# Optimization experiments

Measured on AMD Instinct MI355X. Metric: run time of the kernel, lower is better.

## Reference

```python
import jax, jax.numpy as jnp
import numpy as np

D_MODEL = 1024
N_HEADS = 16
HEAD_DIM = D_MODEL // N_HEADS


def _rotary_tables(seq_len, dim):
    # sin/cos tables: (seq_len, dim//2)
    pos = jnp.arange(seq_len, dtype=jnp.float32)[:, None]
    freqs = 1.0 / 10000.0 ** (jnp.arange(0, dim, 2, dtype=jnp.float32) / dim)
    angles = pos * freqs
    return jnp.sin(angles), jnp.cos(angles)


def _apply_rotary(x, sin, cos):
    # x: (B, H, N, head_dim); sin/cos: (N, head_dim//2) broadcast over B,H
    d_half = x.shape[-1] // 2
    x1, x2 = x[..., :d_half], x[..., d_half:]
    return jnp.concatenate([x1 * cos - x2 * sin, x1 * sin + x2 * cos], axis=-1)


def setup_inputs() -> dict:
    key = jax.random.key(0)
    k_x, k_q, k_k, k_v, k_o = jax.random.split(key, 5)
    B, N = 4, 2048
    scale = 1.0 / np.sqrt(D_MODEL)
    return {
        "x": jax.random.normal(k_x, (B, N, D_MODEL), dtype=jnp.float32),
        "Wq": jax.random.normal(k_q, (D_MODEL, D_MODEL), dtype=jnp.float32) * scale,
        "Wk": jax.random.normal(k_k, (D_MODEL, D_MODEL), dtype=jnp.float32) * scale,
        "Wv": jax.random.normal(k_v, (D_MODEL, D_MODEL), dtype=jnp.float32) * scale,
        "Wo": jax.random.normal(k_o, (D_MODEL, D_MODEL), dtype=jnp.float32) * scale,
    }


def reference(x, Wq, Wk, Wv, Wo):
    B, N, _ = x.shape
    # nn.Linear(d, d, bias=False): y = x @ W.T ; view+transpose -> (B, H, N, hd)
    def proj(W):
        return jnp.einsum('bnd,ed->bne', x, W).reshape(B, N, N_HEADS, HEAD_DIM).transpose(0, 2, 1, 3)

    Q, K, V = proj(Wq), proj(Wk), proj(Wv)
    sin, cos = _rotary_tables(N, HEAD_DIM)
    Q = _apply_rotary(Q, sin, cos)
    K = _apply_rotary(K, sin, cos)

    # SDPA (non-causal, dropout=0): softmax(Q K^T / sqrt(hd)) V
    scores = jnp.einsum('bhqd,bhkd->bhqk', Q, K) / jnp.sqrt(jnp.asarray(HEAD_DIM, x.dtype))
    attn = jax.nn.softmax(scores, axis=-1)
    out = jnp.einsum('bhqk,bhkd->bhqd', attn, V)  # (B, H, N, hd)
    out = out.transpose(0, 2, 1, 3).reshape(B, N, D_MODEL)
    return jnp.einsum('bnd,ed->bne', out, Wo)
```

## Files before the change

kernel.cpp:

```cpp
#include <hip/hip_runtime.h>
#include <stdint.h>

#define SEQ    2048
#define DMODEL 1024
#define NHEADS 16
#define HDIM   64
#define BATCH  4
#define MTOT   (BATCH*SEQ)

typedef __attribute__((ext_vector_type(8)))  short s16x8;
typedef __attribute__((ext_vector_type(4)))  short s16x4;
typedef __attribute__((ext_vector_type(4)))  float f32x4;
typedef __attribute__((ext_vector_type(16))) float f32x16;

#define OFF_SIN  ((size_t)0)
#define OFF_COS  ((size_t)262144)
#define OFF_XHI  ((size_t)524288)
#define OFF_WQH  ((size_t)34078720)
#define OFF_WKH  ((size_t)38273024)
#define OFF_WVH  ((size_t)42467328)
#define OFF_WOH  ((size_t)46661632)
#define OFF_QR   ((size_t)50855936)
#define OFF_KR   ((size_t)67633152)
#define OFF_VT   ((size_t)84410368)
#define OFF_AHI  ((size_t)101187584)

#define QSCALE 0.18033688011112042f

__device__ __forceinline__ uint16_t f2bf(float f){
  union{float f;uint32_t u;}v; v.f=f;
  uint32_t r=v.u+0x7fffu+((v.u>>16)&1u);
  return (uint16_t)(r>>16);
}
__device__ __forceinline__ float bf2f(uint16_t u){
  union{uint32_t u;float f;}v; v.u=((uint32_t)u)<<16; return v.f;
}

__device__ __forceinline__ void async16(void* lds, const void* g){
  __builtin_amdgcn_global_load_lds(
    (const __attribute__((address_space(1))) void*)g,
    (__attribute__((address_space(3))) void*)lds, 16, 0, 0);
}

__device__ __forceinline__ float fexp2(float x){
#if __has_builtin(__builtin_amdgcn_exp2f)
  return __builtin_amdgcn_exp2f(x);
#else
  float r; asm("v_exp_f32 %0, %1" : "=v"(r) : "v"(x)); return r;
#endif
}
__device__ __forceinline__ float frcp(float x){
#if __has_builtin(__builtin_amdgcn_rcpf)
  return __builtin_amdgcn_rcpf(x);
#else
  float r; asm("v_rcp_f32 %0, %1" : "=v"(r) : "v"(x)); return r;
#endif
}
__device__ __forceinline__ void plswap(unsigned a, unsigned b, unsigned &o0, unsigned &o1){
#if __has_builtin(__builtin_amdgcn_permlane32_swap)
  auto r = __builtin_amdgcn_permlane32_swap(a, b, false, false);
  o0 = (unsigned)r[0]; o1 = (unsigned)r[1];
#else
  unsigned ax = (unsigned)__shfl_xor((int)a, 32, 64);
  unsigned bx = (unsigned)__shfl_xor((int)b, 32, 64);
  bool hi = (threadIdx.x & 32) != 0;
  o0 = hi ? bx : a;
  o1 = hi ? b  : ax;
#endif
}

__global__ __launch_bounds__(256) void prep_k(
  const float* __restrict__ x,
  const float* __restrict__ Wq, const float* __restrict__ Wk,
  const float* __restrict__ Wv, const float* __restrict__ Wo,
  uint16_t* __restrict__ xhi, uint16_t* __restrict__ wqh, uint16_t* __restrict__ wkh,
  uint16_t* __restrict__ wvh, uint16_t* __restrict__ woh,
  float* __restrict__ st, float* __restrict__ ct)
{
  int b = blockIdx.x;
  if (b < 12288){
    const float* s; uint16_t* d; int i;
    if (b < 8192){ s = x; d = xhi; i = b*256 + threadIdx.x; }
    else {
      int wsel = (b - 8192) >> 10;
      int lb   = (b - 8192) & 1023;
      s = wsel==0? Wq : wsel==1? Wk : wsel==2? Wv : Wo;
      d = wsel==0? wqh: wsel==1? wkh: wsel==2? wvh: woh;
      i = lb*256 + threadIdx.x;
    }
    f32x4 v = *(const f32x4*)(s + (size_t)i*4);
    s16x4 vh;
    #pragma unroll
    for(int r=0;r<4;r++) vh[r] = (short)f2bf(v[r]);
    *(s16x4*)(d + (size_t)i*4) = vh;
  } else {
    int i = (b - 12288)*256 + threadIdx.x;
    int n = i>>5, j = i&31;
    float freq = powf(10000.f, -(float)j/32.f);
    float ang = (float)n*freq;
    st[i] = sinf(ang);
    ct[i] = cosf(ang);
  }
}

__device__ __forceinline__ void gemm_mainloop64(
  const uint16_t* __restrict__ A, const uint16_t* __restrict__ B,
  int m0, int e0, char* lA, char* lB, f32x4 acc[4][4])
{
  const int t = threadIdx.x;
  const int lane = t & 63;
  const int wr = t>>7, wc = (t>>6)&1;
  const int lq = lane&15, lg = lane>>4;
  const int rowA = wr*64 + lq;
  const int rowB = wc*64 + lq;

  int dbyte[4], srow[4], sbyte[4];
  #pragma unroll
  for (int s=0;s<4;s++){
    int d = s*4096 + t*16;
    int r = d>>7, c = (d>>4)&7;
    dbyte[s]=d; srow[s]=r; sbyte[s]=(c ^ (r&7))*16;
  }
  int chh[2];
  #pragma unroll
  for (int kh=0;kh<2;kh++) chh[kh] = (((kh<<2)|lg) ^ (lq&7))*16;
  const bool oddw = ((t>>6) & 1) != 0;
  const int cF = oddw ? chh[1] : chh[0];
  const int cS = oddw ? chh[0] : chh[1];

  const char* Ab = (const char*)A;
  const char* Bb = (const char*)B;

  for (int k0=0; k0<DMODEL; k0+=64){
    #pragma unroll
    for (int s=0;s<4;s++){
      async16(lA + dbyte[s], Ab + (size_t)(m0+srow[s])*2048 + k0*2 + sbyte[s]);
      async16(lB + dbyte[s], Bb + (size_t)(e0+srow[s])*2048 + k0*2 + sbyte[s]);
    }
    __syncthreads();
    #pragma unroll
    for (int ph=0; ph<2; ++ph){
      const int ch = ph ? cS : cF;
      s16x8 af[4], bfr[4];
      #pragma unroll
      for (int mi=0;mi<4;mi++) af[mi]  = *(const s16x8*)(lA + (rowA+mi*16)*128 + ch);
      #pragma unroll
      for (int ni=0;ni<4;ni++) bfr[ni] = *(const s16x8*)(lB + (rowB+ni*16)*128 + ch);
      __builtin_amdgcn_s_setprio(1);
      #pragma unroll
      for (int mi=0;mi<4;mi++){
        #pragma unroll
        for (int ni=0;ni<4;ni++)
          acc[mi][ni] = __builtin_amdgcn_mfma_f32_16x16x32_bf16(af[mi], bfr[ni], acc[mi][ni],0,0,0);
      }
      __builtin_amdgcn_s_setprio(0);
    }
    __syncthreads();
  }
}

__global__ __launch_bounds__(256) void gemm_qkv_k(
  const uint16_t* __restrict__ Xh,
  const uint16_t* __restrict__ WqH, const uint16_t* __restrict__ WkH, const uint16_t* __restrict__ WvH,
  const float* __restrict__ st, const float* __restrict__ ct,
  uint16_t* __restrict__ Qr, uint16_t* __restrict__ Kr, uint16_t* __restrict__ Vt)
{
  __shared__ char lA[128*128], lB[128*128];
  int mx = blockIdx.x;
  int m0 = (((mx & 7) << 3) | (mx >> 3)) * 128;
  int cti = blockIdx.y;
  int seg = cti>>3;
  int e0 = (cti&7)*128;
  const uint16_t* W = seg==0? WqH : (seg==1? WkH : WvH);
  f32x4 acc[4][4];
  #pragma unroll
  for(int i=0;i<4;i++){
    #pragma unroll
    for(int j=0;j<4;j++) acc[i][j] = (f32x4){0.f,0.f,0.f,0.f};
  }
  gemm_mainloop64(Xh, W, m0, e0, lA, lB, acc);

  int t=threadIdx.x, lane=t&63, lq=lane&15, lg=lane>>4;
  int wr=t>>7, wc=(t>>6)&1;
  int eb = e0 + wc*64;
  int h = eb>>6;
  int rbase = m0 + wr*64 + lg*4;
  if (seg<2){
    uint16_t* O = seg==0? Qr:Kr;
    float qs = seg==0 ? QSCALE : 1.0f;
    #pragma unroll
    for(int mi=0;mi<4;mi++){
      #pragma unroll
      for(int ni=0;ni<2;ni++){
        int j = ni*16+lq;
        #pragma unroll
        for(int r=0;r<4;r++){
          int m = rbase + mi*16 + r;
          int b = m>>11, n = m&2047;
          float sv = st[n*32+j], cv = ct[n*32+j];
          float x1 = acc[mi][ni][r], x2 = acc[mi][ni+2][r];
          size_t base = ((size_t)((b*NHEADS+h)*SEQ + n))*HDIM;
          O[base + j]      = f2bf((x1*cv - x2*sv)*qs);
          O[base + j + 32] = f2bf((x1*sv + x2*cv)*qs);
        }
      }
    }
  } else {
    #pragma unroll
    for(int mi=0;mi<4;mi++){
      #pragma unroll
      for(int ni=0;ni<4;ni++){
        int dh = ni*16+lq;
        int m = rbase + mi*16;
        int b = m>>11, n = m&2047;
        s16x4 v;
        #pragma unroll
        for(int r=0;r<4;r++) v[r] = (short)f2bf(acc[mi][ni][r]);
        *(s16x4*)(Vt + ((size_t)((b*NHEADS+h)*HDIM + dh))*SEQ + n) = v;
      }
    }
  }
}

__global__ __launch_bounds__(512) void attn_k(
  const uint16_t* __restrict__ Qr, const uint16_t* __restrict__ Kr, const uint16_t* __restrict__ Vt,
  uint16_t* __restrict__ Ah)
{
  __shared__ char lds[32768];

  int bid = blockIdx.x;
  int w = (bid & 7)*64 + (bid >> 3);
  int bh = w >> 3, qt = w & 7;
  int tid = threadIdx.x;
  int wid = tid >> 6, lane = tid & 63;
  int l31 = lane & 31, hi = lane >> 5;
  int q0 = qt*256 + wid*32;

  const uint16_t* Qb = Qr + (size_t)bh*SEQ*HDIM;
  const uint16_t* Kb = Kr + (size_t)bh*SEQ*HDIM;
  const uint16_t* Vb = Vt + (size_t)bh*HDIM*SEQ;

  s16x8 qf[4];
  #pragma unroll
  for (int sp=0; sp<4; ++sp)
    qf[sp] = *(const s16x8*)(Qb + (size_t)(q0 + l31)*HDIM + sp*16 + hi*8);

  s16x8 ones;
  #pragma unroll
  for (int j=0;j<8;j++) ones[j] = (short)0x3F80;

  f32x16 zm16;
  #pragma unroll
  for (int r=0;r<16;r++) zm16[r] = -16.0f;

  f32x16 oa[2], lacc;
  #pragma unroll
  for (int r=0;r<16;r++){ oa[0][r]=0.f; oa[1][r]=0.f; lacc[r]=0.f; }

  const int e7 = l31 & 7;
  const int rK = l31*128;
  const int kOff[4]  = { (((0+hi)^e7)<<4), (((2+hi)^e7)<<4), (((4+hi)^e7)<<4), (((6+hi)^e7)<<4) };
  const int vA0 = (((0+hi)^e7)<<4), vA1 = (((2+hi)^e7)<<4);
  const int vB0 = (((4+hi)^e7)<<4), vB1 = (((6+hi)^e7)<<4);
  const bool odd = (wid & 1) != 0;
  const int kBaseF = odd ? 4096 : 0,   kBaseS = odd ? 0 : 4096;
  const int vF0 = odd ? vB0 : vA0,     vF1 = odd ? vB1 : vA1;
  const int vS0 = odd ? vA0 : vB0,     vS1 = odd ? vA1 : vB1;

  auto STAGE = [&](int buf, int t){
    const char* Ks = (const char*)(Kb + (size_t)t*64*HDIM);
    char* dK = lds + buf*8192;
    char* dV = lds + 16384 + buf*8192;
    {
      int ci = tid;
      int sc = ci ^ ((ci>>3)&7);
      async16(dK + ci*16, Ks + sc*16);
    }
    {
      int ci = tid;
      int row = ci>>3;
      int sc = (ci&7) ^ (row&7);
      async16(dV + ci*16, (const char*)Vb + ((size_t)row*SEQ + (size_t)t*64)*2 + sc*16);
    }
  };

  auto SUBSTEP = [&](const char* bK, const char* bV, int kbase, int v0, int v1){
    s16x8 kf[4];
    #pragma unroll
    for (int sp=0; sp<4; ++sp)
      kf[sp] = *(const s16x8*)(bK + kbase + rK + kOff[sp]);
    f32x16 sacc = zm16;
    __builtin_amdgcn_s_setprio(1);
    #pragma unroll
    for (int sp=0; sp<4; ++sp)
      sacc = __builtin_amdgcn_mfma_f32_32x32x16_bf16(kf[sp], qf[sp], sacc, 0,0,0);
    __builtin_amdgcn_s_setprio(0);
    s16x8 vf[4];
    #pragma unroll
    for (int db=0; db<2; ++db){
      vf[db*2+0] = *(const s16x8*)(bV + db*4096 + rK + v0);
      vf[db*2+1] = *(const s16x8*)(bV + db*4096 + rK + v1);
    }
    float p[16];
    #pragma unroll
    for (int r=0;r<16;r++) p[r] = fexp2(sacc[r]);
    uint32_t pw[8];
    #pragma unroll
    for (int j=0;j<8;j++)
      asm("v_cvt_pk_bf16_f32 %0, %1, %2" : "=v"(pw[j]) : "v"(p[2*j]), "v"(p[2*j+1]));
    unsigned w0,w1,w2,w3, x0,x1,x2,x3;
    plswap(pw[0], pw[2], w0, w2);
    plswap(pw[1], pw[3], w1, w3);
    plswap(pw[4], pw[6], x0, x2);
    plswap(pw[5], pw[7], x1, x3);
    union { uint32_t wd[4]; s16x8 v; } pa0, pa1;
    pa0.wd[0]=w0; pa0.wd[1]=w1; pa0.wd[2]=w2; pa0.wd[3]=w3;
    pa1.wd[0]=x0; pa1.wd[1]=x1; pa1.wd[2]=x2; pa1.wd[3]=x3;
    __builtin_amdgcn_s_setprio(1);
    oa[0] = __builtin_amdgcn_mfma_f32_32x32x16_bf16(pa0.v, vf[0], oa[0], 0,0,0);
    oa[0] = __builtin_amdgcn_mfma_f32_32x32x16_bf16(pa1.v, vf[1], oa[0], 0,0,0);
    oa[1] = __builtin_amdgcn_mfma_f32_32x32x16_bf16(pa0.v, vf[2], oa[1], 0,0,0);
    oa[1] = __builtin_amdgcn_mfma_f32_32x32x16_bf16(pa1.v, vf[3], oa[1], 0,0,0);
    lacc = __builtin_amdgcn_mfma_f32_32x32x16_bf16(pa0.v, ones, lacc, 0,0,0);
    lacc = __builtin_amdgcn_mfma_f32_32x32x16_bf16(pa1.v, ones, lacc, 0,0,0);
    __builtin_amdgcn_s_setprio(0);
  };

  STAGE(0, 0);
  asm volatile("s_waitcnt vmcnt(0)" ::: "memory");
  __syncthreads();

  const int NT = SEQ/64;
  for (int t=0; t<NT; ++t){
    int cur = t & 1;
    if (t+1 < NT) STAGE(cur^1, t+1);
    const char* bK = lds + cur*8192;
    const char* bV = lds + 16384 + cur*8192;
    SUBSTEP(bK, bV, kBaseF, vF0, vF1);
    SUBSTEP(bK, bV, kBaseS, vS0, vS1);
    asm volatile("s_waitcnt vmcnt(0)" ::: "memory");
    __syncthreads();
  }

  int b = bh >> 4, h = bh & 15;
  #pragma unroll
  for (int r=0;r<16;r++){
    int q = (r&3) + 8*(r>>2) + 4*hi;
    float inv = frcp(lacc[r]);
    size_t mrow = ((size_t)(b*SEQ + q0 + q))*DMODEL + (size_t)h*HDIM + l31;
    #pragma unroll
    for (int db=0; db<2; ++db)
      Ah[mrow + db*32] = f2bf(oa[db][r]*inv);
  }
}

__global__ __launch_bounds__(256) void gemm_out_k(
  const uint16_t* __restrict__ Ahp, const uint16_t* __restrict__ WoH, float* __restrict__ C)
{
  __shared__ char lA[128*128], lB[128*128];
  int mx = blockIdx.x;
  int m0 = (((mx & 7) << 3) | (mx >> 3)) * 128;
  int e0 = blockIdx.y*128;
  f32x4 acc[4][4];
  #pragma unroll
  for(int i=0;i<4;i++){
    #pragma unroll
    for(int j=0;j<4;j++) acc[i][j] = (f32x4){0.f,0.f,0.f,0.f};
  }
  gemm_mainloop64(Ahp, WoH, m0, e0, lA, lB, acc);
  int t=threadIdx.x, lane=t&63, lq=lane&15, lg=lane>>4;
  int wr=t>>7, wc=(t>>6)&1;
  int rbase = m0 + wr*64 + lg*4;
  int cb = e0 + wc*64;
  #pragma unroll
  for(int mi=0;mi<4;mi++){
    #pragma unroll
    for(int ni=0;ni<4;ni++){
      #pragma unroll
      for(int r=0;r<4;r++)
        C[(size_t)(rbase+mi*16+r)*DMODEL + cb + ni*16 + lq] = acc[mi][ni][r];
    }
  }
}

extern "C" void kernel_launch(void* const* d_in, const int* in_sizes, int n_in,
                              void* d_out, int out_size, void* d_ws, size_t ws_size,
                              hipStream_t stream) {
  const float* x  = (const float*)d_in[0];
  const float* Wq = (const float*)d_in[1];
  const float* Wk = (const float*)d_in[2];
  const float* Wv = (const float*)d_in[3];
  const float* Wo = (const float*)d_in[4];
  float* out = (float*)d_out;
  char* ws = (char*)d_ws;

  float* sin_t = (float*)(ws + OFF_SIN);
  float* cos_t = (float*)(ws + OFF_COS);
  uint16_t* xhi = (uint16_t*)(ws + OFF_XHI);
  uint16_t* wqh = (uint16_t*)(ws + OFF_WQH);
  uint16_t* wkh = (uint16_t*)(ws + OFF_WKH);
  uint16_t* wvh = (uint16_t*)(ws + OFF_WVH);
  uint16_t* woh = (uint16_t*)(ws + OFF_WOH);
  uint16_t* Qr  = (uint16_t*)(ws + OFF_QR);
  uint16_t* Kr  = (uint16_t*)(ws + OFF_KR);
  uint16_t* Vt  = (uint16_t*)(ws + OFF_VT);
  uint16_t* ahi = (uint16_t*)(ws + OFF_AHI);

  prep_k<<<dim3(12544),dim3(256),0,stream>>>(x, Wq, Wk, Wv, Wo,
                                             xhi, wqh, wkh, wvh, woh, sin_t, cos_t);

  gemm_qkv_k<<<dim3(MTOT/128, 24),dim3(256),0,stream>>>(xhi, wqh, wkh, wvh,
                                                        sin_t, cos_t, Qr, Kr, Vt);
  attn_k<<<dim3(BATCH*NHEADS*(SEQ/256)),dim3(512),0,stream>>>(Qr, Kr, Vt, ahi);
  gemm_out_k<<<dim3(MTOT/128, 8),dim3(256),0,stream>>>(ahi, woh, out);
}
```

Baseline: 183.0 us.

## Double attention block size to 1024 threads and split K/V staging across threads

The attention kernel now uses 1024-thread blocks covering 512 queries each, so every K/V tile staged in LDS is shared by 16 waves instead of 8. That halves global K/V traffic per query. The staging work is split so the first 512 threads load K and the rest load V, with pointers computed once and advanced per tile. The trade-off is a block-wide barrier over twice as many waves and a launch_bounds hint of 4 blocks per CU, which may cap registers and limit occupancy.

```diff
diff --git a/kernel.cpp b/kernel.cpp
--- a/kernel.cpp
+++ b/kernel.cpp
@@ -222,19 +222,19 @@
   }
 }
 
-__global__ __launch_bounds__(512) void attn_k(
+__global__ __launch_bounds__(1024, 4) void attn_k(
   const uint16_t* __restrict__ Qr, const uint16_t* __restrict__ Kr, const uint16_t* __restrict__ Vt,
   uint16_t* __restrict__ Ah)
 {
   __shared__ char lds[32768];
 
   int bid = blockIdx.x;
-  int w = (bid & 7)*64 + (bid >> 3);
-  int bh = w >> 3, qt = w & 7;
+  int w = (bid & 7)*32 + (bid >> 3);
+  int bh = w >> 2, qt = w & 3;
   int tid = threadIdx.x;
   int wid = tid >> 6, lane = tid & 63;
   int l31 = lane & 31, hi = lane >> 5;
-  int q0 = qt*256 + wid*32;
+  int q0 = qt*512 + wid*32;
 
   const uint16_t* Qb = Qr + (size_t)bh*SEQ*HDIM;
   const uint16_t* Kb = Kr + (size_t)bh*SEQ*HDIM;
@@ -267,22 +267,19 @@
   const int vF0 = odd ? vB0 : vA0,     vF1 = odd ? vB1 : vA1;
   const int vS0 = odd ? vA0 : vB0,     vS1 = odd ? vA1 : vB1;
 
-  auto STAGE = [&](int buf, int t){
-    const char* Ks = (const char*)(Kb + (size_t)t*64*HDIM);
-    char* dK = lds + buf*8192;
-    char* dV = lds + 16384 + buf*8192;
-    {
-      int ci = tid;
-      int sc = ci ^ ((ci>>3)&7);
-      async16(dK + ci*16, Ks + sc*16);
-    }
-    {
-      int ci = tid;
-      int row = ci>>3;
-      int sc = (ci&7) ^ (row&7);
-      async16(dV + ci*16, (const char*)Vb + ((size_t)row*SEQ + (size_t)t*64)*2 + sc*16);
-    }
-  };
+  const bool isK = (tid < 512);
+  const int ci = isK ? tid : (tid - 512);
+  const int sck = ci ^ ((ci>>3)&7);
+  const int rowv = ci>>3;
+  const int scv = (ci&7) ^ (rowv&7);
+  const char* src = isK ? ((const char*)Kb + sck*16)
+                        : ((const char*)Vb + (size_t)rowv*4096 + scv*16);
+  const ptrdiff_t sstep = isK ? 8192 : 128;
+  char* const dst0 = lds + (isK ? ci*16 : 16384 + ci*16);
+
+  async16(dst0, src); src += sstep;
+  asm volatile("s_waitcnt vmcnt(0)" ::: "memory");
+  __syncthreads();
 
   auto SUBSTEP = [&](const char* bK, const char* bV, int kbase, int v0, int v1){
     s16x8 kf[4];
@@ -326,14 +323,13 @@
     __builtin_amdgcn_s_setprio(0);
   };
 
-  STAGE(0, 0);
-  asm volatile("s_waitcnt vmcnt(0)" ::: "memory");
-  __syncthreads();
-
   const int NT = SEQ/64;
   for (int t=0; t<NT; ++t){
     int cur = t & 1;
-    if (t+1 < NT) STAGE(cur^1, t+1);
+    if (t+1 < NT){
+      async16(dst0 + (cur^1)*8192, src);
+      src += sstep;
+    }
     const char* bK = lds + cur*8192;
     const char* bV = lds + 16384 + cur*8192;
     SUBSTEP(bK, bV, kBaseF, vF0, vF1);
@@ -411,6 +407,6 @@
 
   gemm_qkv_k<<<dim3(MTOT/128, 24),dim3(256),0,stream>>>(xhi, wqh, wkh, wvh,
                                                         sin_t, cos_t, Qr, Kr, Vt);
-  attn_k<<<dim3(BATCH*NHEADS*(SEQ/256)),dim3(512),0,stream>>>(Qr, Kr, Vt, ahi);
+  attn_k<<<dim3(BATCH*NHEADS*(SEQ/512)),dim3(1024),0,stream>>>(Qr, Kr, Vt, ahi);
   gemm_out_k<<<dim3(MTOT/128, 8),dim3(256),0,stream>>>(ahi, woh, out);
 }
```

New measurement: 192.9 us. 5.4% more time.
